# Optimization experiments

Hardware: AMD Instinct MI355X
Metric: run time of the kernel (lower is better)

Reference implementation:

```python
import jax, jax.numpy as jnp
import numpy as np

N = 4_000_000
TAU = 1.0
LOSS_WEIGHT = 1.0
EPS = 1e-6


def _xy_wh_r_2_xy_sigma_components(xywhr):
    """Convert [N,5] (x,y,w,h,r) boxes to mu [N,2] and 2x2 sigma components.

    sigma = R diag((w/2)^2, (h/2)^2) R^T, returned as (s11, s12, s22) [N] each.
    """
    xy = xywhr[..., :2]
    wh = jnp.clip(xywhr[..., 2:4], 1e-7, 1e7)
    r = xywhr[..., 4]
    c, s = jnp.cos(r), jnp.sin(r)
    a = (0.5 * wh[..., 0]) ** 2  # (w/2)^2
    b = (0.5 * wh[..., 1]) ** 2  # (h/2)^2
    s11 = a * c * c + b * s * s
    s12 = (a - b) * s * c
    s22 = a * s * s + b * c * c
    return xy, s11, s12, s22


def setup_inputs() -> dict:
    key = jax.random.key(0)
    k1, k2 = jax.random.split(key)

    def rand_boxes(k):
        kx, kw, kr = jax.random.split(k, 3)
        xy = jax.random.normal(kx, (N, 2), dtype=jnp.float32) * 10.0
        wh = jax.random.uniform(kw, (N, 2), minval=2.0, maxval=50.0, dtype=jnp.float32)
        r = jax.random.uniform(kr, (N, 1), minval=-np.pi, maxval=np.pi, dtype=jnp.float32)
        return jnp.concatenate([xy, wh, r], axis=-1)

    pred = rand_boxes(k1)
    target = rand_boxes(k2)
    weight = jnp.ones((N,), dtype=jnp.float32)  # all > 0 -> mask keeps all boxes
    return {"pred": pred, "target": target, "weight": weight}


def reference(pred, target, weight):
    # mask = weight > 0 is all-True for weight=ones, so pred[mask] == pred.
    mu_p, p11, p12, p22 = _xy_wh_r_2_xy_sigma_components(pred)
    mu_t, t11, t12, t22 = _xy_wh_r_2_xy_sigma_components(target)

    det_p = p11 * p22 - p12 * p12
    det_t = t11 * t22 - t12 * t12

    dx = mu_p[..., 0] - mu_t[..., 0]
    dy = mu_p[..., 1] - mu_t[..., 1]

    # delta^T Sigma_t^{-1} delta (closed-form 2x2 inverse)
    term1 = (t22 * dx * dx - 2.0 * t12 * dx * dy + t11 * dy * dy) / det_t
    # trace(Sigma_t^{-1} Sigma_p) + log(det Sigma_t / det Sigma_p)
    trace_term = (t22 * p11 - 2.0 * t12 * p12 + t11 * p22) / det_t
    term2 = trace_term + jnp.log(det_t / det_p)

    dis = term1 + term2 - 2.0
    kl_dis = jnp.clip(dis, EPS)
    # fun='sqrt'
    loss = 1.0 - 1.0 / (TAU + jnp.sqrt(kl_dis))
    return loss[:, None] * LOSS_WEIGHT  # [N,1] matching torch keepdim layout
```

## Files before the change

### kernel.cpp

```cpp
#include <hip/hip_runtime.h>
#include <math.h>

#define EPS 1e-6f
#define TAU 1.0f

__device__ __forceinline__ float box_loss(float px, float py, float pw, float ph, float pr,
                                          float tx, float ty, float tw, float th, float tr) {
    pw = fminf(fmaxf(pw, 1e-7f), 1e7f);
    ph = fminf(fmaxf(ph, 1e-7f), 1e7f);
    tw = fminf(fmaxf(tw, 1e-7f), 1e7f);
    th = fminf(fmaxf(th, 1e-7f), 1e7f);

    float pa = 0.25f * pw * pw, pb = 0.25f * ph * ph;
    float ta = 0.25f * tw * tw, tb = 0.25f * th * th;

    float ps, pc, ts, tc;
    __sincosf(pr, &ps, &pc);
    __sincosf(tr, &ts, &tc);

    float p11 = pa * pc * pc + pb * ps * ps;
    float p12 = (pa - pb) * ps * pc;
    float p22 = pa * ps * ps + pb * pc * pc;
    float t11 = ta * tc * tc + tb * ts * ts;
    float t12 = (ta - tb) * ts * tc;
    float t22 = ta * ts * ts + tb * tc * tc;

    float det_p = p11 * p22 - p12 * p12;
    float det_t = t11 * t22 - t12 * t12;

    float dx = px - tx;
    float dy = py - ty;

    float inv_det_t = __frcp_rn(det_t);
    float term1 = (t22 * dx * dx - 2.0f * t12 * dx * dy + t11 * dy * dy) * inv_det_t;
    float trace_term = (t22 * p11 - 2.0f * t12 * p12 + t11 * p22) * inv_det_t;
    float term2 = trace_term + __logf(det_t) - __logf(det_p);

    float dis = term1 + term2 - 2.0f;
    float kl = fmaxf(dis, EPS);
    return 1.0f - __frcp_rn(TAU + sqrtf(kl));
}

__global__ void __launch_bounds__(256) gd_loss_kernel4(
        const float4* __restrict__ pred4,
        const float4* __restrict__ tgt4,
        float4* __restrict__ out4, int n4) {
    int i = blockIdx.x * blockDim.x + threadIdx.x;
    if (i >= n4) return;

    const float4* p = pred4 + (size_t)i * 5;
    const float4* t = tgt4  + (size_t)i * 5;

    float4 a0 = p[0], a1 = p[1], a2 = p[2], a3 = p[3], a4 = p[4];
    float4 b0 = t[0], b1 = t[1], b2 = t[2], b3 = t[3], b4 = t[4];

    float4 r;
    r.x = box_loss(a0.x, a0.y, a0.z, a0.w, a1.x,
                   b0.x, b0.y, b0.z, b0.w, b1.x);
    r.y = box_loss(a1.y, a1.z, a1.w, a2.x, a2.y,
                   b1.y, b1.z, b1.w, b2.x, b2.y);
    r.z = box_loss(a2.z, a2.w, a3.x, a3.y, a3.z,
                   b2.z, b2.w, b3.x, b3.y, b3.z);
    r.w = box_loss(a3.w, a4.x, a4.y, a4.z, a4.w,
                   b3.w, b4.x, b4.y, b4.z, b4.w);

    out4[i] = r;
}

__global__ void __launch_bounds__(64) gd_loss_tail(
        const float* __restrict__ pred,
        const float* __restrict__ tgt,
        float* __restrict__ out, int start, int n) {
    int i = start + blockIdx.x * blockDim.x + threadIdx.x;
    if (i >= n) return;
    const float* p = pred + (size_t)i * 5;
    const float* t = tgt  + (size_t)i * 5;
    out[i] = box_loss(p[0], p[1], p[2], p[3], p[4],
                      t[0], t[1], t[2], t[3], t[4]);
}

extern "C" void kernel_launch(void* const* d_in, const int* in_sizes, int n_in,
                              void* d_out, int out_size, void* d_ws, size_t ws_size,
                              hipStream_t stream) {
    const float* pred = (const float*)d_in[0];
    const float* tgt  = (const float*)d_in[1];
    float* out = (float*)d_out;
    int n = out_size;

    int n4 = n >> 2;
    int rem = n & 3;

    if (n4 > 0) {
        int block = 256;
        int grid = (n4 + block - 1) / block;
        gd_loss_kernel4<<<grid, block, 0, stream>>>(
            (const float4*)pred, (const float4*)tgt, (float4*)out, n4);
    }
    if (rem > 0) {
        gd_loss_tail<<<1, 64, 0, stream>>>(pred, tgt, out, n4 << 2, n);
    }
}
```

Measured before the change: 186.7 us.

## Stage box data through LDS with coalesced float4 loads, one box per thread

Replaces the per-thread 5×float4 strided loads (four boxes per thread) with a block-cooperative coalesced float4 load of 256 boxes into shared memory, after which each thread computes one box. The goal is to fix the uncoalesced 80-byte stride access pattern of the old kernel. In exchange it adds LDS traffic, a barrier, bank conflicts from the stride-5 reads, and one scalar output store per thread instead of float4 stores. It also launches four times as many threads.

```diff
diff --git a/kernel.cpp b/kernel.cpp
--- a/kernel.cpp
+++ b/kernel.cpp
@@ -41,42 +41,45 @@
     return 1.0f - __frcp_rn(TAU + sqrtf(kl));
 }
 
-__global__ void __launch_bounds__(256) gd_loss_kernel4(
-        const float4* __restrict__ pred4,
-        const float4* __restrict__ tgt4,
-        float4* __restrict__ out4, int n4) {
-    int i = blockIdx.x * blockDim.x + threadIdx.x;
-    if (i >= n4) return;
-
-    const float4* p = pred4 + (size_t)i * 5;
-    const float4* t = tgt4  + (size_t)i * 5;
-
-    float4 a0 = p[0], a1 = p[1], a2 = p[2], a3 = p[3], a4 = p[4];
-    float4 b0 = t[0], b1 = t[1], b2 = t[2], b3 = t[3], b4 = t[4];
-
-    float4 r;
-    r.x = box_loss(a0.x, a0.y, a0.z, a0.w, a1.x,
-                   b0.x, b0.y, b0.z, b0.w, b1.x);
-    r.y = box_loss(a1.y, a1.z, a1.w, a2.x, a2.y,
-                   b1.y, b1.z, b1.w, b2.x, b2.y);
-    r.z = box_loss(a2.z, a2.w, a3.x, a3.y, a3.z,
-                   b2.z, b2.w, b3.x, b3.y, b3.z);
-    r.w = box_loss(a3.w, a4.x, a4.y, a4.z, a4.w,
-                   b3.w, b4.x, b4.y, b4.z, b4.w);
-
-    out4[i] = r;
-}
-
-__global__ void __launch_bounds__(64) gd_loss_tail(
+__global__ void __launch_bounds__(256) gd_loss_lds(
         const float* __restrict__ pred,
         const float* __restrict__ tgt,
-        float* __restrict__ out, int start, int n) {
-    int i = start + blockIdx.x * blockDim.x + threadIdx.x;
+        float* __restrict__ out, int n) {
+    __shared__ float sp[1280];
+    __shared__ float st[1280];
+
+    const int b = blockIdx.x;
+    const int t = threadIdx.x;
+    const size_t fbase = (size_t)b * 1280;
+    const size_t nf = (size_t)n * 5;
+
+    #pragma unroll
+    for (int k = t; k < 320; k += 256) {
+        size_t f = fbase + (size_t)k * 4;
+        if (f + 3 < nf) {
+            float4 vp = *reinterpret_cast<const float4*>(pred + f);
+            float4 vt = *reinterpret_cast<const float4*>(tgt + f);
+            *reinterpret_cast<float4*>(sp + k * 4) = vp;
+            *reinterpret_cast<float4*>(st + k * 4) = vt;
+        } else {
+            for (int j = 0; j < 4; ++j) {
+                size_t f2 = f + j;
+                if (f2 < nf) {
+                    sp[k * 4 + j] = pred[f2];
+                    st[k * 4 + j] = tgt[f2];
+                }
+            }
+        }
+    }
+    __syncthreads();
+
+    int i = b * 256 + t;
     if (i >= n) return;
-    const float* p = pred + (size_t)i * 5;
-    const float* t = tgt  + (size_t)i * 5;
+
+    const float* p = sp + t * 5;
+    const float* q = st + t * 5;
     out[i] = box_loss(p[0], p[1], p[2], p[3], p[4],
-                      t[0], t[1], t[2], t[3], t[4]);
+                      q[0], q[1], q[2], q[3], q[4]);
 }
 
 extern "C" void kernel_launch(void* const* d_in, const int* in_sizes, int n_in,
@@ -87,16 +90,7 @@
     float* out = (float*)d_out;
     int n = out_size;
 
-    int n4 = n >> 2;
-    int rem = n & 3;
-
-    if (n4 > 0) {
-        int block = 256;
-        int grid = (n4 + block - 1) / block;
-        gd_loss_kernel4<<<grid, block, 0, stream>>>(
-            (const float4*)pred, (const float4*)tgt, (float4*)out, n4);
-    }
-    if (rem > 0) {
-        gd_loss_tail<<<1, 64, 0, stream>>>(pred, tgt, out, n4 << 2, n);
-    }
+    int block = 256;
+    int grid = (n + block - 1) / block;
+    gd_loss_lds<<<grid, block, 0, stream>>>(pred, tgt, out, n);
 }
```

Measured after the change: 185.4 us. No clear change (-0.7%).

## Persistent double-buffered LDS pipeline using async global_load_lds tile staging

Applied to the files above, without the earlier changes.

Replaces the one-thread-per-four-boxes kernel with a persistent kernel of 1024 blocks. Each block walks 512-box tiles and stages the next tile of pred and target into a second LDS buffer with the global-to-LDS DMA builtin, while it computes the current tile from the first. The goal is to overlap memory traffic with the transcendental-heavy compute and to keep wide coalesced loads without per-thread register staging. In exchange it adds LDS use, a barrier per tile, and dependence on the wait semantics of the async LDS loads. It also adds an odd `t11*t12*0.0f` term to det_t, which looks like a compiler-scheduling trick and can turn infinities into NaN.

```diff
diff --git a/kernel.cpp b/kernel.cpp
--- a/kernel.cpp
+++ b/kernel.cpp
@@ -3,6 +3,10 @@
 
 #define EPS 1e-6f
 #define TAU 1.0f
+
+#define TILE_BOXES 512
+#define TILE_F4    640
+#define NBLOCKS    1024
 
 __device__ __forceinline__ float box_loss(float px, float py, float pw, float ph, float pr,
                                           float tx, float ty, float tw, float th, float tr) {
@@ -26,7 +30,7 @@
     float t22 = ta * ts * ts + tb * tc * tc;
 
     float det_p = p11 * p22 - p12 * p12;
-    float det_t = t11 * t22 - t12 * t12;
+    float det_t = t11 * t12 * 0.0f + t11 * t22 - t12 * t12;
 
     float dx = px - tx;
     float dy = py - ty;
@@ -41,30 +45,57 @@
     return 1.0f - __frcp_rn(TAU + sqrtf(kl));
 }
 
-__global__ void __launch_bounds__(256) gd_loss_kernel4(
+__global__ void __launch_bounds__(256) gd_loss_pipe(
         const float4* __restrict__ pred4,
         const float4* __restrict__ tgt4,
-        float4* __restrict__ out4, int n4) {
-    int i = blockIdx.x * blockDim.x + threadIdx.x;
-    if (i >= n4) return;
+        float* __restrict__ out, int ntiles) {
+    __shared__ float sp[2][TILE_BOXES * 5];
+    __shared__ float st[2][TILE_BOXES * 5];
 
-    const float4* p = pred4 + (size_t)i * 5;
-    const float4* t = tgt4  + (size_t)i * 5;
+    const int t = threadIdx.x;
 
-    float4 a0 = p[0], a1 = p[1], a2 = p[2], a3 = p[3], a4 = p[4];
-    float4 b0 = t[0], b1 = t[1], b2 = t[2], b3 = t[3], b4 = t[4];
+    auto stage = [&](int buf, int tile) {
+        const float4* ps = pred4 + (size_t)tile * TILE_F4;
+        const float4* ts = tgt4  + (size_t)tile * TILE_F4;
+        #pragma unroll
+        for (int k = t; k < TILE_F4; k += 256) {
+            __builtin_amdgcn_global_load_lds(
+                (const __attribute__((address_space(1))) void*)(ps + k),
+                (__attribute__((address_space(3))) void*)(&sp[buf][k * 4]),
+                16, 0, 0);
+            __builtin_amdgcn_global_load_lds(
+                (const __attribute__((address_space(1))) void*)(ts + k),
+                (__attribute__((address_space(3))) void*)(&st[buf][k * 4]),
+                16, 0, 0);
+        }
+    };
 
-    float4 r;
-    r.x = box_loss(a0.x, a0.y, a0.z, a0.w, a1.x,
-                   b0.x, b0.y, b0.z, b0.w, b1.x);
-    r.y = box_loss(a1.y, a1.z, a1.w, a2.x, a2.y,
-                   b1.y, b1.z, b1.w, b2.x, b2.y);
-    r.z = box_loss(a2.z, a2.w, a3.x, a3.y, a3.z,
-                   b2.z, b2.w, b3.x, b3.y, b3.z);
-    r.w = box_loss(a3.w, a4.x, a4.y, a4.z, a4.w,
-                   b3.w, b4.x, b4.y, b4.z, b4.w);
+    int tile = blockIdx.x;
+    if (tile >= ntiles) return;
 
-    out4[i] = r;
+    stage(0, tile);
+    __syncthreads();
+
+    int buf = 0;
+    while (true) {
+        int nxt = tile + NBLOCKS;
+        if (nxt < ntiles) stage(buf ^ 1, nxt);
+
+        #pragma unroll
+        for (int k = 0; k < 2; ++k) {
+            int b = t + k * 256;
+            const float* p = &sp[buf][b * 5];
+            const float* q = &st[buf][b * 5];
+            out[(size_t)tile * TILE_BOXES + b] =
+                box_loss(p[0], p[1], p[2], p[3], p[4],
+                         q[0], q[1], q[2], q[3], q[4]);
+        }
+
+        if (nxt >= ntiles) break;
+        __syncthreads();
+        buf ^= 1;
+        tile = nxt;
+    }
 }
 
 __global__ void __launch_bounds__(64) gd_loss_tail(
@@ -87,16 +118,16 @@
     float* out = (float*)d_out;
     int n = out_size;
 
-    int n4 = n >> 2;
-    int rem = n & 3;
+    int ntiles = n / TILE_BOXES;
+    int rem = n - ntiles * TILE_BOXES;
 
-    if (n4 > 0) {
-        int block = 256;
-        int grid = (n4 + block - 1) / block;
-        gd_loss_kernel4<<<grid, block, 0, stream>>>(
-            (const float4*)pred, (const float4*)tgt, (float4*)out, n4);
+    if (ntiles > 0) {
+        int grid = ntiles < NBLOCKS ? ntiles : NBLOCKS;
+        gd_loss_pipe<<<grid, 256, 0, stream>>>(
+            (const float4*)pred, (const float4*)tgt, out, ntiles);
     }
     if (rem > 0) {
-        gd_loss_tail<<<1, 64, 0, stream>>>(pred, tgt, out, n4 << 2, n);
+        int grid = (rem + 63) / 64;
+        gd_loss_tail<<<grid, 64, 0, stream>>>(pred, tgt, out, ntiles * TILE_BOXES, n);
     }
 }
```

Measured after the change: 190.8 us. 2.2% more time.
